# Kernel optimization log

Hardware: AMD Instinct MI355X
Metric: run time of the kernel (lower is better)

## Reference

```python
import jax, jax.numpy as jnp
import numpy as np

BASE = 257
HASH_MOD = 4096
WINDOWS = (2, 4, 8, 16)
MATCH_OFFSETS = (1, 2, 4, 8)
CHUNK = 32
EPS_LN = 1e-5


def _shift_right(x, k):
    # (B,T) -> shifted right by k along time, zero-filled
    B, T = x.shape
    return jnp.concatenate([jnp.zeros((B, k), x.dtype), x[:, :T - k]], axis=1)


def _rolling_hashes(chars):
    # polynomial rolling hash over each window size, mod HASH_MOD -> (B,T,S) int32
    c = chars.astype(jnp.int32)
    hs = []
    for w in WINDOWS:
        acc = jnp.zeros_like(c)
        p = 1
        for j in range(w):  # small fixed loop (<=16)
            acc = acc + _shift_right(c, j) * p
            p = (p * BASE) % HASH_MOD
        hs.append(acc % HASH_MOD)
    return jnp.stack(hs, axis=2)


def _match_features(chars):
    feats = []
    for k in MATCH_OFFSETS:
        m = (chars == _shift_right(chars, k)).astype(jnp.float32)
        m = m.at[:, :k].set(0.0)
        feats.append(m)
    return jnp.stack(feats, axis=-1)  # (B,T,n_match)


def _layer_norm(x, g, b):
    mu = jnp.mean(x, axis=-1, keepdims=True)
    var = jnp.mean((x - mu) ** 2, axis=-1, keepdims=True)
    return (x - mu) * jax.lax.rsqrt(var + EPS_LN) * g + b


def _forward(chars, emb_byte, hash_tables, Wq, bq, conv_w, conv_b, Win, b_in,
             Wg, bg, Wi, bi, Wo, bo, ln_g, ln_b, mlp_w, mlp_b, Wout, bout):
    B, T = chars.shape
    byte_emb = emb_byte[chars]                       # (B,T,Eb)
    hidx = _rolling_hashes(chars)                    # (B,T,S)
    scale_embeds = jnp.stack(
        [hash_tables[s][hidx[:, :, s]] for s in range(len(WINDOWS))], axis=2
    )                                                # (B,T,S,E)
    # scale attention: query from byte embedding, softmax over scales
    E = scale_embeds.shape[-1]
    q = byte_emb @ Wq + bq                           # (B,T,E)
    scores = jnp.einsum('bte,btse->bts', q, scale_embeds) / jnp.sqrt(jnp.float32(E))
    w = jax.nn.softmax(scores, axis=-1)
    hash_feat = jnp.einsum('bts,btse->bte', w, scale_embeds)
    # causal depthwise conv + silu
    C = hash_feat.shape[-1]
    kk = conv_w.shape[-1]
    ht = jnp.moveaxis(hash_feat, 1, 2)               # (B,C,T)
    ht = jnp.pad(ht, ((0, 0), (0, 0), (kk - 1, 0)))
    ht = jax.lax.conv_general_dilated(
        ht, conv_w, window_strides=(1,), padding='VALID',
        dimension_numbers=('NCH', 'OIH', 'NCH'), feature_group_count=C)
    hash_feat = jax.nn.silu(jnp.moveaxis(ht + conv_b[None, :, None], 2, 1))
    mf = _match_features(chars)
    feat = jnp.concatenate([byte_emb, hash_feat, mf], axis=-1)
    h = jax.nn.silu(feat @ Win + b_in)               # (B,T,H)
    # TinyScan: chunked log-space gated scan, carry across chunks via lax.scan
    gates = jax.nn.sigmoid(h @ Wg + bg)              # (B,T,S)
    drive = (1.0 - gates) * (h @ Wi + bi)
    S = gates.shape[-1]
    nC = T // CHUNK
    g = gates.reshape(B, nC, CHUNK, S).transpose(1, 0, 2, 3)
    d = drive.reshape(B, nC, CHUNK, S).transpose(1, 0, 2, 3)

    def step(hc, ab):
        a, b = ab                                    # (B,K,S)
        log_a = jnp.log(jnp.maximum(a, 1e-6))
        cum_a = jnp.exp(jnp.cumsum(log_a, axis=1))
        inv = 1.0 / jnp.maximum(cum_a, 1e-8)
        cum_wb = jnp.cumsum(b * inv, axis=1)
        out = cum_a * (hc[:, None, :] + cum_wb)
        return out[:, -1], out

    _, states = jax.lax.scan(step, jnp.zeros((B, S), h.dtype), (g, d))
    states = states.transpose(1, 0, 2, 3).reshape(B, T, S)
    h = _layer_norm(h + states @ Wo + bo, ln_g, ln_b)
    # residual MLP blocks: x + silu(Linear(x))
    for l in range(mlp_w.shape[0]):
        h = h + jax.nn.silu(h @ mlp_w[l] + mlp_b[l])
    return h @ Wout + bout                           # (B,T,V)


def setup_inputs() -> dict:
    key = jax.random.key(0)
    ks = jax.random.split(key, 12)
    B, T, V = 8, 8192, 256
    EB, E, H, SS, KC, NM, NR = 64, 64, 512, 32, 4, 4, 3
    feat = EB + E + NM

    def lin(k, i, o):
        return (jax.random.normal(k, (i, o), jnp.float32) / np.sqrt(i)).astype(jnp.float32)

    return {
        'chars': jax.random.randint(ks[0], (B, T), 0, V),
        'emb_byte': jax.random.normal(ks[1], (V, EB), jnp.float32) * 0.02,
        'hash_tables': jax.random.normal(ks[2], (len(WINDOWS), HASH_MOD, E), jnp.float32) * 0.02,
        'Wq': lin(ks[3], EB, E), 'bq': jnp.zeros((E,), jnp.float32),
        'conv_w': jax.random.normal(ks[4], (E, 1, KC), jnp.float32) * 0.2,
        'conv_b': jnp.zeros((E,), jnp.float32),
        'Win': lin(ks[5], feat, H), 'b_in': jnp.zeros((H,), jnp.float32),
        'Wg': lin(ks[6], H, SS), 'bg': jnp.zeros((SS,), jnp.float32),
        'Wi': lin(ks[7], H, SS), 'bi': jnp.zeros((SS,), jnp.float32),
        'Wo': lin(ks[8], SS, H), 'bo': jnp.zeros((H,), jnp.float32),
        'ln_g': jnp.ones((H,), jnp.float32), 'ln_b': jnp.zeros((H,), jnp.float32),
        'mlp_w': jax.random.normal(ks[9], (NR, H, H), jnp.float32) / np.sqrt(H),
        'mlp_b': jnp.zeros((NR, H), jnp.float32),
        'Wout': lin(ks[10], H, V), 'bout': jnp.zeros((V,), jnp.float32),
    }


def reference(chars, emb_byte, hash_tables, Wq, bq, conv_w, conv_b, Win, b_in,
              Wg, bg, Wi, bi, Wo, bo, ln_g, ln_b, mlp_w, mlp_b, Wout, bout):
    return _forward(chars, emb_byte, hash_tables, Wq, bq, conv_w, conv_b, Win, b_in,
                    Wg, bg, Wi, bi, Wo, bo, ln_g, ln_b, mlp_w, mlp_b, Wout, bout)
```

## Files before the change

### kernel.cpp

```cpp
#include <hip/hip_runtime.h>
#include <hip/hip_bf16.h>
#include <math.h>

#define B_ 8
#define T_ 8192
#define V_ 256
#define EB_ 64
#define E_ 64
#define H_ 512
#define SS_ 32
#define FEATP_ 192
#define NCH_ 256
#define CHUNK_ 32

typedef __attribute__((ext_vector_type(8))) short bf8;
typedef __attribute__((ext_vector_type(16))) float accv;

#define AS1(p) (__attribute__((address_space(1))) void*)(void*)(p)
#define AS3(p) (__attribute__((address_space(3))) void*)(void*)(p)

__device__ __forceinline__ float silu_f(float x) { return x / (1.0f + expf(-x)); }
__device__ __forceinline__ float sigm_f(float x) { return 1.0f / (1.0f + expf(-x)); }
__device__ __forceinline__ float bf2f(__hip_bfloat16 v) { return __bfloat162float(v); }
__device__ __forceinline__ __hip_bfloat16 f2bf(float v) { return __float2bfloat16(v); }
__device__ __forceinline__ float us2f(ushort u) {
    union { float f; unsigned int u32; } c; c.u32 = ((unsigned int)u) << 16; return c.f;
}
__device__ __forceinline__ ushort f2us(float v) {
    __hip_bfloat16 t = __float2bfloat16(v);
    return *reinterpret_cast<ushort*>(&t);
}

#define CD_ROW(r, lane) (((r) & 3) + 8 * ((r) >> 2) + 4 * ((lane) >> 5))

__device__ __forceinline__ int xcd_swz(int bid, int nwg) {
    return (bid & 7) * (nwg >> 3) + (bid >> 3);
}

template <int KD>
__device__ __forceinline__ void mm256(const ushort* __restrict__ Ab,
                                      const ushort* __restrict__ Bb,
                                      int m0, int n0, accv (&acc)[4][2]) {
    constexpr int NT = KD / 64;
    __shared__ __align__(1024) ushort lA[33280];
    __shared__ __align__(1024) ushort lB[33280];
    const int tid  = threadIdx.x;
    const int lane = tid & 63;
    const int w    = tid >> 6;
    const int wm   = w >> 2, wn = w & 3;
    const int l31  = lane & 31, lh = lane >> 5;

    const int srow = lane >> 3;
    const int scg  = (lane & 7) ^ ((srow & 1) << 2);
    const ushort* gA = Ab + (size_t)(m0 + w * 32 + srow) * KD + scg * 8;
    const ushort* gB = Bb + (size_t)(n0 + w * 32 + srow) * KD + scg * 8;
    const int dgrp = w * 4;

    const int rbase = (l31 >> 3) * 520 + (l31 & 7) * 64;
    int oK[4];
#pragma unroll
    for (int ks = 0; ks < 4; ks++) oK[ks] = (((ks * 2 + lh) ^ ((l31 & 1) << 2)) << 3);
    const int aoff = wm * 8320 + rbase;
    const int boff = wn * 4160 + rbase;

#define STG8(slot, kt)                                                                             \
    do {                                                                                           \
        __builtin_amdgcn_global_load_lds(AS1(gA + (kt)),                                           \
                                         AS3(&lA[(slot) * 16640 + (dgrp + 0) * 520]), 16, 0, 0);   \
        __builtin_amdgcn_global_load_lds(AS1(gB + (kt)),                                           \
                                         AS3(&lB[(slot) * 16640 + (dgrp + 0) * 520]), 16, 0, 0);   \
        __builtin_amdgcn_global_load_lds(AS1(gA + (size_t)8 * KD + (kt)),                          \
                                         AS3(&lA[(slot) * 16640 + (dgrp + 1) * 520]), 16, 0, 0);   \
        __builtin_amdgcn_global_load_lds(AS1(gB + (size_t)8 * KD + (kt)),                          \
                                         AS3(&lB[(slot) * 16640 + (dgrp + 1) * 520]), 16, 0, 0);   \
        __builtin_amdgcn_global_load_lds(AS1(gA + (size_t)16 * KD + (kt)),                         \
                                         AS3(&lA[(slot) * 16640 + (dgrp + 2) * 520]), 16, 0, 0);   \
        __builtin_amdgcn_global_load_lds(AS1(gB + (size_t)16 * KD + (kt)),                         \
                                         AS3(&lB[(slot) * 16640 + (dgrp + 2) * 520]), 16, 0, 0);   \
        __builtin_amdgcn_global_load_lds(AS1(gA + (size_t)24 * KD + (kt)),                         \
                                         AS3(&lA[(slot) * 16640 + (dgrp + 3) * 520]), 16, 0, 0);   \
        __builtin_amdgcn_global_load_lds(AS1(gB + (size_t)24 * KD + (kt)),                         \
                                         AS3(&lB[(slot) * 16640 + (dgrp + 3) * 520]), 16, 0, 0);   \
    } while (0)

#define PH(slot, ks)                                                                               \
    do {                                                                                           \
        const ushort* pa = &lA[(slot) * 16640 + aoff + oK[ks]];                                    \
        const ushort* pb = &lB[(slot) * 16640 + boff + oK[ks]];                                    \
        bf8 b0v = *(const bf8*)(pb);                                                               \
        bf8 b1v = *(const bf8*)(pb + 2080);                                                        \
        bf8 a0v = *(const bf8*)(pa);                                                               \
        bf8 a1v = *(const bf8*)(pa + 2080);                                                        \
        bf8 a2v = *(const bf8*)(pa + 4160);                                                        \
        bf8 a3v = *(const bf8*)(pa + 6240);                                                        \
        acc[0][0] = __builtin_amdgcn_mfma_f32_32x32x16_bf16(a0v, b0v, acc[0][0], 0, 0, 0);         \
        acc[0][1] = __builtin_amdgcn_mfma_f32_32x32x16_bf16(a0v, b1v, acc[0][1], 0, 0, 0);         \
        acc[1][0] = __builtin_amdgcn_mfma_f32_32x32x16_bf16(a1v, b0v, acc[1][0], 0, 0, 0);         \
        acc[1][1] = __builtin_amdgcn_mfma_f32_32x32x16_bf16(a1v, b1v, acc[1][1], 0, 0, 0);         \
        acc[2][0] = __builtin_amdgcn_mfma_f32_32x32x16_bf16(a2v, b0v, acc[2][0], 0, 0, 0);         \
        acc[2][1] = __builtin_amdgcn_mfma_f32_32x32x16_bf16(a2v, b1v, acc[2][1], 0, 0, 0);         \
        acc[3][0] = __builtin_amdgcn_mfma_f32_32x32x16_bf16(a3v, b0v, acc[3][0], 0, 0, 0);         \
        acc[3][1] = __builtin_amdgcn_mfma_f32_32x32x16_bf16(a3v, b1v, acc[3][1], 0, 0, 0);         \
    } while (0)

    STG8(0, 0);
#pragma unroll
    for (int t = 0; t < NT - 1; ++t) {
        const int slot = t & 1;
        STG8(slot ^ 1, (t + 1) * 64);
        asm volatile("s_waitcnt vmcnt(8)" ::: "memory");
        __builtin_amdgcn_s_barrier();
        __builtin_amdgcn_sched_barrier(0);
        __builtin_amdgcn_s_setprio(1);
        PH(slot, 0); PH(slot, 1); PH(slot, 2); PH(slot, 3);
        __builtin_amdgcn_s_setprio(0);
        __builtin_amdgcn_s_barrier();
    }
    asm volatile("s_waitcnt vmcnt(0)" ::: "memory");
    __builtin_amdgcn_s_barrier();
    __builtin_amdgcn_sched_barrier(0);
    {
        const int ls = (NT - 1) & 1;
        __builtin_amdgcn_s_setprio(1);
        PH(ls, 0); PH(ls, 1); PH(ls, 2); PH(ls, 3);
        __builtin_amdgcn_s_setprio(0);
    }
#undef STG8
#undef PH
}

__device__ __forceinline__ void zero_acc8(accv (&acc)[4][2]) {
#pragma unroll
    for (int i = 0; i < 4; i++)
#pragma unroll
        for (int j = 0; j < 2; j++)
#pragma unroll
            for (int r = 0; r < 16; r++) acc[i][j][r] = 0.0f;
}

__global__ __launch_bounds__(512, 2) void k_mlp256(const __hip_bfloat16* __restrict__ hin,
                                                   const __hip_bfloat16* __restrict__ Wt,
                                                   const float* __restrict__ bias,
                                                   __hip_bfloat16* __restrict__ hout) {
    accv acc[4][2];
    zero_acc8(acc);
    int wg = xcd_swz(blockIdx.x, 512);
    int m0 = (wg >> 1) * 256, n0 = (wg & 1) * 256;
    int lane = threadIdx.x & 63, w = threadIdx.x >> 6, wm = w >> 2, wn = w & 3;
    mm256<H_>((const ushort*)hin, (const ushort*)Wt, m0, n0, acc);
#pragma unroll
    for (int fr = 0; fr < 4; fr++)
#pragma unroll
        for (int fc = 0; fc < 2; fc++) {
            int col = n0 + 64 * wn + 32 * fc + (lane & 31);
            float bv = bias[col];
#pragma unroll
            for (int r = 0; r < 16; r++) {
                int row = m0 + 128 * wm + 32 * fr + CD_ROW(r, lane);
                float v = acc[fr][fc][r] + bv;
                float res = bf2f(hin[(size_t)row * H_ + col]);
                hout[(size_t)row * H_ + col] = f2bf(res + silu_f(v));
            }
        }
}

__global__ __launch_bounds__(512, 2) void k_win256(const __hip_bfloat16* __restrict__ featb,
                                                   const __hip_bfloat16* __restrict__ Wt,
                                                   const float* __restrict__ bias,
                                                   __hip_bfloat16* __restrict__ hb) {
    accv acc[4][2];
    zero_acc8(acc);
    int wg = xcd_swz(blockIdx.x, 512);
    int m0 = (wg >> 1) * 256, n0 = (wg & 1) * 256;
    int lane = threadIdx.x & 63, w = threadIdx.x >> 6, wm = w >> 2, wn = w & 3;
    mm256<FEATP_>((const ushort*)featb, (const ushort*)Wt, m0, n0, acc);
#pragma unroll
    for (int fr = 0; fr < 4; fr++)
#pragma unroll
        for (int fc = 0; fc < 2; fc++) {
            int col = n0 + 64 * wn + 32 * fc + (lane & 31);
            float bv = bias[col];
#pragma unroll
            for (int r = 0; r < 16; r++) {
                int row = m0 + 128 * wm + 32 * fr + CD_ROW(r, lane);
                hb[(size_t)row * H_ + col] = f2bf(silu_f(acc[fr][fc][r] + bv));
            }
        }
}

__global__ __launch_bounds__(512, 2) void k_out256(const __hip_bfloat16* __restrict__ hb,
                                                   const __hip_bfloat16* __restrict__ Wt,
                                                   const float* __restrict__ bout,
                                                   float* __restrict__ out) {
    accv acc[4][2];
    zero_acc8(acc);
    int wg = xcd_swz(blockIdx.x, 256);
    int m0 = wg * 256;
    int lane = threadIdx.x & 63, w = threadIdx.x >> 6, wm = w >> 2, wn = w & 3;
    mm256<H_>((const ushort*)hb, (const ushort*)Wt, m0, 0, acc);
#pragma unroll
    for (int fr = 0; fr < 4; fr++)
#pragma unroll
        for (int fc = 0; fc < 2; fc++) {
            int col = 64 * wn + 32 * fc + (lane & 31);
            float bv = bout[col];
#pragma unroll
            for (int r = 0; r < 16; r++) {
                int row = m0 + 128 * wm + 32 * fr + CD_ROW(r, lane);
                out[(size_t)row * V_ + col] = acc[fr][fc][r] + bv;
            }
        }
}

template <int KD>
__device__ __forceinline__ void mm128(const __hip_bfloat16* __restrict__ A,
                                      const __hip_bfloat16* __restrict__ Wt,
                                      int m0, int n0, accv (&acc)[2][2]) {
    __shared__ __align__(16) ushort lA[128 * 32];
    __shared__ __align__(16) ushort lB[128 * 32];
    int tid = threadIdx.x;
    int lane = tid & 63, w = tid >> 6;
    int wm = w & 1, wn = w >> 1;
    int c0 = w * 128 + lane;
    int c1 = c0 + 64;
    const ushort* Ab = (const ushort*)A;
    const ushort* Bb = (const ushort*)Wt;
    const ushort* gA0 = Ab + (size_t)(m0 + (c0 >> 2)) * KD + (c0 & 3) * 8;
    const ushort* gA1 = Ab + (size_t)(m0 + (c1 >> 2)) * KD + (c1 & 3) * 8;
    const ushort* gB0 = Bb + (size_t)(n0 + (c0 >> 2)) * KD + (c0 & 3) * 8;
    const ushort* gB1 = Bb + (size_t)(n0 + (c1 >> 2)) * KD + (c1 & 3) * 8;
    ushort* dA0 = &lA[(w * 128) * 8];
    ushort* dA1 = &lA[(w * 128 + 64) * 8];
    ushort* dB0 = &lB[(w * 128) * 8];
    ushort* dB1 = &lB[(w * 128 + 64) * 8];
    const ushort* pa = &lA[(64 * wm + (lane & 31)) * 32 + (lane >> 5) * 8];
    const ushort* pb = &lB[(64 * wn + (lane & 31)) * 32 + (lane >> 5) * 8];

    for (int kt = 0; kt < KD; kt += 32) {
        __builtin_amdgcn_global_load_lds(AS1(gA0 + kt), AS3(dA0), 16, 0, 0);
        __builtin_amdgcn_global_load_lds(AS1(gA1 + kt), AS3(dA1), 16, 0, 0);
        __builtin_amdgcn_global_load_lds(AS1(gB0 + kt), AS3(dB0), 16, 0, 0);
        __builtin_amdgcn_global_load_lds(AS1(gB1 + kt), AS3(dB1), 16, 0, 0);
        __syncthreads();
#pragma unroll
        for (int ks = 0; ks < 2; ks++) {
            bf8 a0 = *(const bf8*)(pa + ks * 16);
            bf8 a1 = *(const bf8*)(pa + 32 * 32 + ks * 16);
            bf8 b0 = *(const bf8*)(pb + ks * 16);
            bf8 b1 = *(const bf8*)(pb + 32 * 32 + ks * 16);
            acc[0][0] = __builtin_amdgcn_mfma_f32_32x32x16_bf16(a0, b0, acc[0][0], 0, 0, 0);
            acc[0][1] = __builtin_amdgcn_mfma_f32_32x32x16_bf16(a0, b1, acc[0][1], 0, 0, 0);
            acc[1][0] = __builtin_amdgcn_mfma_f32_32x32x16_bf16(a1, b0, acc[1][0], 0, 0, 0);
            acc[1][1] = __builtin_amdgcn_mfma_f32_32x32x16_bf16(a1, b1, acc[1][1], 0, 0, 0);
        }
        __syncthreads();
    }
}

__device__ __forceinline__ void zero_acc(accv (&acc)[2][2]) {
#pragma unroll
    for (int i = 0; i < 2; i++)
#pragma unroll
        for (int j = 0; j < 2; j++)
#pragma unroll
            for (int r = 0; r < 16; r++) acc[i][j][r] = 0.0f;
}

__global__ __launch_bounds__(256) void k_womm(const __hip_bfloat16* __restrict__ states_bf,
                                              const __hip_bfloat16* __restrict__ Wt_wo,
                                              const float* __restrict__ bo,
                                              const __hip_bfloat16* __restrict__ hb,
                                              __hip_bfloat16* __restrict__ tmp) {
    accv acc[2][2];
    zero_acc(acc);
    int lane = threadIdx.x & 63, w = threadIdx.x >> 6, wm = w & 1, wn = w >> 1;
    int m0 = blockIdx.x * 128, n0 = blockIdx.y * 128;
    mm128<SS_>(states_bf, Wt_wo, m0, n0, acc);
#pragma unroll
    for (int i = 0; i < 2; i++)
#pragma unroll
        for (int j = 0; j < 2; j++) {
            int col = n0 + 64 * wn + 32 * j + (lane & 31);
            float bv = bo[col];
#pragma unroll
            for (int r = 0; r < 16; r++) {
                int row = m0 + 64 * wm + 32 * i + CD_ROW(r, lane);
                float res = bf2f(hb[(size_t)row * H_ + col]);
                tmp[(size_t)row * H_ + col] = f2bf(res + acc[i][j][r] + bv);
            }
        }
}

__global__ __launch_bounds__(256) void k_ln(const __hip_bfloat16* __restrict__ tmp,
                                            const float* __restrict__ ln_g,
                                            const float* __restrict__ ln_b,
                                            __hip_bfloat16* __restrict__ hb) {
    int wave = threadIdx.x >> 6, lane = threadIdx.x & 63;
    int token = blockIdx.x * 4 + wave;
    const ushort* row = (const ushort*)(tmp + (size_t)token * H_) + lane * 8;
    bf8 xv = *(const bf8*)row;
    float x[8];
    float sm = 0.f, sq = 0.f;
#pragma unroll
    for (int i = 0; i < 8; i++) {
        x[i] = us2f((ushort)xv[i]);
        sm += x[i];
        sq += x[i] * x[i];
    }
#pragma unroll
    for (int off = 32; off; off >>= 1) {
        sm += __shfl_xor(sm, off, 64);
        sq += __shfl_xor(sq, off, 64);
    }
    float mu = sm * (1.0f / 512.0f);
    float var = sq * (1.0f / 512.0f) - mu * mu;
    float rstd = rsqrtf(fmaxf(var, 0.0f) + 1e-5f);
    float4 g0 = *(const float4*)(ln_g + lane * 8);
    float4 g1 = *(const float4*)(ln_g + lane * 8 + 4);
    float4 b0 = *(const float4*)(ln_b + lane * 8);
    float4 b1 = *(const float4*)(ln_b + lane * 8 + 4);
    float gg[8] = {g0.x, g0.y, g0.z, g0.w, g1.x, g1.y, g1.z, g1.w};
    float bb[8] = {b0.x, b0.y, b0.z, b0.w, b1.x, b1.y, b1.z, b1.w};
    bf8 o;
#pragma unroll
    for (int i = 0; i < 8; i++) o[i] = (short)f2us((x[i] - mu) * rstd * gg[i] + bb[i]);
    *(bf8*)((ushort*)(hb + (size_t)token * H_) + lane * 8) = o;
}

__global__ __launch_bounds__(256) void k_gates_mfma(const __hip_bfloat16* __restrict__ hb,
                                                    const __hip_bfloat16* __restrict__ Wt_gd,
                                                    const float* __restrict__ bg,
                                                    const float* __restrict__ bi,
                                                    float* __restrict__ gates,
                                                    float* __restrict__ drive) {
    __shared__ __align__(16) ushort lA[256 * 32];
    __shared__ __align__(16) ushort lB[64 * 32];
    int tid = threadIdx.x, lane = tid & 63, w = tid >> 6;
    int m0 = blockIdx.x * 256;
    accv acc[2][2];
    zero_acc(acc);
    const ushort* Ab = (const ushort*)hb;
    const ushort* Bb = (const ushort*)Wt_gd;
    const ushort* pa = &lA[(64 * w + (lane & 31)) * 32 + (lane >> 5) * 8];
    const ushort* pb = &lB[((lane & 31)) * 32 + (lane >> 5) * 8];
    int cb = w * 64 + lane;
    const ushort* gB = Bb + (size_t)(cb >> 2) * H_ + (cb & 3) * 8;
    for (int kt = 0; kt < H_; kt += 32) {
#pragma unroll
        for (int j = 0; j < 4; j++) {
            int c = w * 256 + j * 64 + lane;
            __builtin_amdgcn_global_load_lds(
                AS1(Ab + (size_t)(m0 + (c >> 2)) * H_ + (c & 3) * 8 + kt),
                AS3(&lA[(w * 256 + j * 64) * 8]), 16, 0, 0);
        }
        __builtin_amdgcn_global_load_lds(AS1(gB + kt), AS3(&lB[(w * 64) * 8]), 16, 0, 0);
        __syncthreads();
#pragma unroll
        for (int ks = 0; ks < 2; ks++) {
            bf8 a0 = *(const bf8*)(pa + ks * 16);
            bf8 a1 = *(const bf8*)(pa + 32 * 32 + ks * 16);
            bf8 b0 = *(const bf8*)(pb + ks * 16);
            bf8 b1 = *(const bf8*)(pb + 32 * 32 + ks * 16);
            acc[0][0] = __builtin_amdgcn_mfma_f32_32x32x16_bf16(a0, b0, acc[0][0], 0, 0, 0);
            acc[0][1] = __builtin_amdgcn_mfma_f32_32x32x16_bf16(a0, b1, acc[0][1], 0, 0, 0);
            acc[1][0] = __builtin_amdgcn_mfma_f32_32x32x16_bf16(a1, b0, acc[1][0], 0, 0, 0);
            acc[1][1] = __builtin_amdgcn_mfma_f32_32x32x16_bf16(a1, b1, acc[1][1], 0, 0, 0);
        }
        __syncthreads();
    }
    int c = lane & 31;
    float bgv = bg[c], biv = bi[c];
#pragma unroll
    for (int i = 0; i < 2; i++)
#pragma unroll
        for (int r = 0; r < 16; r++) {
            int row = m0 + 64 * w + 32 * i + CD_ROW(r, lane);
            float g = sigm_f(acc[i][0][r] + bgv);
            float d = (1.0f - g) * (acc[i][1][r] + biv);
            gates[(size_t)row * SS_ + c] = g;
            drive[(size_t)row * SS_ + c] = d;
        }
}

__global__ __launch_bounds__(256) void k_prep_w(const float* __restrict__ mlp_w,
                                                const float* __restrict__ Wout,
                                                const float* __restrict__ Win,
                                                const float* __restrict__ Wg,
                                                const float* __restrict__ Wi,
                                                const float* __restrict__ Wo,
                                                const float* __restrict__ Wq,
                                                const float* __restrict__ bq,
                                                const float* __restrict__ emb_byte,
                                                __hip_bfloat16* __restrict__ Wt_mlp,
                                                __hip_bfloat16* __restrict__ Wt_out,
                                                __hip_bfloat16* __restrict__ Wt_win,
                                                __hip_bfloat16* __restrict__ Wt_gd,
                                                __hip_bfloat16* __restrict__ Wt_wo,
                                                float* __restrict__ Qtab) {
    int idx = blockIdx.x * 256 + threadIdx.x;
    if (idx < 786432) {
        int l = idx >> 18, rem = idx & 262143;
        int n = rem >> 9, k = rem & 511;
        Wt_mlp[idx] = f2bf(mlp_w[l * 262144 + k * 512 + n]);
    } else if (idx < 917504) {
        int rem = idx - 786432;
        int n = rem >> 9, k = rem & 511;
        Wt_out[rem] = f2bf(Wout[k * 256 + n]);
    } else if (idx < 1015808) {
        int rem = idx - 917504;
        int n = rem / FEATP_, k = rem % FEATP_;
        Wt_win[rem] = f2bf(k < 132 ? Win[k * 512 + n] : 0.0f);
    } else if (idx < 1048576) {
        int rem = idx - 1015808;
        int n = rem >> 9, k = rem & 511;
        Wt_gd[rem] = f2bf(n < 32 ? Wg[k * 32 + n] : Wi[k * 32 + (n - 32)]);
    } else if (idx < 1064960) {
        int rem = idx - 1048576;
        int n = rem >> 5, k = rem & 31;
        Wt_wo[rem] = f2bf(Wo[k * H_ + n]);
    } else if (idx < 1081344) {
        int rem = idx - 1064960;
        int c = rem >> 6, e = rem & 63;
        float a = bq[e];
#pragma unroll 8
        for (int k = 0; k < 64; k++) a += emb_byte[c * 64 + k] * Wq[k * 64 + e];
        Qtab[rem] = a * 0.125f;
    }
}

__global__ __launch_bounds__(256) void k_token_feats(
    const int* __restrict__ chars, const float* __restrict__ emb_byte,
    const float* __restrict__ hash_tables, const float* __restrict__ Qtab,
    __hip_bfloat16* __restrict__ featb, float* __restrict__ hfpre) {
    int wave = threadIdx.x >> 6, lane = threadIdx.x & 63;
    int token = blockIdx.x * 4 + wave;
    int t = token & (T_ - 1);
    int b = token >> 13;
    const int* crow = chars + b * T_;
    int cv[16];
#pragma unroll
    for (int j = 0; j < 16; j++) cv[j] = (t >= j) ? crow[t - j] : 0;
    int acc = 0;
    int hidx[4];
#pragma unroll
    for (int j = 0; j < 16; j++) {
        acc += cv[j] * (1 + 256 * j);
        if (j == 1) hidx[0] = acc & 4095;
        if (j == 3) hidx[1] = acc & 4095;
        if (j == 7) hidx[2] = acc & 4095;
        if (j == 15) hidx[3] = acc & 4095;
    }
    int c0 = cv[0];
    float be = emb_byte[c0 * EB_ + lane];
    float q = Qtab[c0 * 64 + lane];
    float se[4];
#pragma unroll
    for (int s = 0; s < 4; s++) se[s] = hash_tables[(s * 4096 + hidx[s]) * E_ + lane];
    float sc[4];
#pragma unroll
    for (int s = 0; s < 4; s++) {
        float v = q * se[s];
#pragma unroll
        for (int off = 32; off; off >>= 1) v += __shfl_xor(v, off, 64);
        sc[s] = v;
    }
    float mx = fmaxf(fmaxf(sc[0], sc[1]), fmaxf(sc[2], sc[3]));
    float w0 = expf(sc[0] - mx), w1 = expf(sc[1] - mx), w2 = expf(sc[2] - mx), w3 = expf(sc[3] - mx);
    float inv = 1.0f / (w0 + w1 + w2 + w3);
    float hf = (w0 * se[0] + w1 * se[1] + w2 * se[2] + w3 * se[3]) * inv;
    featb[(size_t)token * FEATP_ + lane] = f2bf(be);
    hfpre[(size_t)token * E_ + lane] = hf;
    if (lane < 32) {
        float m = 0.0f;
        if (lane < 4) {
            int k = 1 << lane;
            m = (t >= k && c0 == cv[k]) ? 1.0f : 0.0f;
        }
        featb[(size_t)token * FEATP_ + 128 + lane] = f2bf(m);
    } else {
        featb[(size_t)token * FEATP_ + 128 + lane] = f2bf(0.0f);
    }
}

__global__ __launch_bounds__(256) void k_conv(
    const float* __restrict__ hfpre, const float* __restrict__ conv_w,
    const float* __restrict__ conv_b, __hip_bfloat16* __restrict__ featb) {
    int idx = blockIdx.x * 256 + threadIdx.x;
    int e = idx & 63;
    int bt = idx >> 6;
    int t = bt & (T_ - 1);
    float acc = conv_b[e];
#pragma unroll
    for (int k = 0; k < 4; k++) {
        int tt = t - 3 + k;
        if (tt >= 0) acc += hfpre[(size_t)(bt - 3 + k) * E_ + e] * conv_w[e * 4 + k];
    }
    featb[(size_t)bt * FEATP_ + 64 + e] = f2bf(silu_f(acc));
}

__global__ __launch_bounds__(256) void k_chunk_ab(
    const float* __restrict__ gates, const float* __restrict__ drive,
    float* __restrict__ chA, float* __restrict__ chB) {
    int gid = blockIdx.x * 256 + threadIdx.x;
    int s = gid & 31;
    int n = (gid >> 5) & (NCH_ - 1);
    int b = gid >> 13;
    int base = (b * T_ + n * CHUNK_) * SS_ + s;
    float suml = 0.f, cum_wb = 0.f, cum_a = 1.f;
    for (int i = 0; i < CHUNK_; i++) {
        float g = gates[base + i * SS_];
        float d = drive[base + i * SS_];
        suml += logf(fmaxf(g, 1e-6f));
        cum_a = expf(suml);
        cum_wb += d / fmaxf(cum_a, 1e-8f);
    }
    chA[gid] = cum_a;
    chB[gid] = cum_a * cum_wb;
}

__global__ void k_chunk_scan(const float* __restrict__ chA, const float* __restrict__ chB,
                             float* __restrict__ chH) {
    int tid = threadIdx.x;
    int b = tid >> 5, s = tid & 31;
    const float* pA = chA + (size_t)b * NCH_ * SS_ + s;
    const float* pB = chB + (size_t)b * NCH_ * SS_ + s;
    float* pH = chH + (size_t)b * NCH_ * SS_ + s;
    float hc = 0.f;
    for (int n = 0; n < NCH_; n += 8) {
        float a[8], bb[8];
#pragma unroll
        for (int i = 0; i < 8; i++) {
            a[i] = pA[(n + i) * SS_];
            bb[i] = pB[(n + i) * SS_];
        }
#pragma unroll
        for (int i = 0; i < 8; i++) {
            pH[(n + i) * SS_] = hc;
            hc = a[i] * hc + bb[i];
        }
    }
}

__global__ __launch_bounds__(256) void k_states(
    const float* __restrict__ gates, const float* __restrict__ drive,
    const float* __restrict__ chH, __hip_bfloat16* __restrict__ states_bf) {
    int gid = blockIdx.x * 256 + threadIdx.x;
    int s = gid & 31;
    int n = (gid >> 5) & (NCH_ - 1);
    int b = gid >> 13;
    int base = (b * T_ + n * CHUNK_) * SS_ + s;
    float hc = chH[gid];
    float suml = 0.f, cum_wb = 0.f;
    for (int i = 0; i < CHUNK_; i++) {
        float g = gates[base + i * SS_];
        float d = drive[base + i * SS_];
        suml += logf(fmaxf(g, 1e-6f));
        float cum_a = expf(suml);
        cum_wb += d / fmaxf(cum_a, 1e-8f);
        states_bf[base + i * SS_] = f2bf(cum_a * (hc + cum_wb));
    }
}

extern "C" void kernel_launch(void* const* d_in, const int* in_sizes, int n_in,
                              void* d_out, int out_size, void* d_ws, size_t ws_size,
                              hipStream_t stream) {
    (void)in_sizes; (void)n_in; (void)out_size; (void)ws_size;
    const int*   chars       = (const int*)  d_in[0];
    const float* emb_byte    = (const float*)d_in[1];
    const float* hash_tables = (const float*)d_in[2];
    const float* Wq          = (const float*)d_in[3];
    const float* bq          = (const float*)d_in[4];
    const float* conv_w      = (const float*)d_in[5];
    const float* conv_b      = (const float*)d_in[6];
    const float* Win         = (const float*)d_in[7];
    const float* b_in        = (const float*)d_in[8];
    const float* Wg          = (const float*)d_in[9];
    const float* bg          = (const float*)d_in[10];
    const float* Wi          = (const float*)d_in[11];
    const float* bi          = (const float*)d_in[12];
    const float* Wo          = (const float*)d_in[13];
    const float* bo          = (const float*)d_in[14];
    const float* ln_g        = (const float*)d_in[15];
    const float* ln_b        = (const float*)d_in[16];
    const float* mlp_w       = (const float*)d_in[17];
    const float* mlp_b       = (const float*)d_in[18];
    const float* Wout        = (const float*)d_in[19];
    const float* bout        = (const float*)d_in[20];
    float* out = (float*)d_out;

    const size_t NTOK = (size_t)B_ * T_;
    char* p = (char*)d_ws;
    auto alloc = [&](size_t bytes) { void* r = (void*)p; p += (bytes + 255) & ~(size_t)255; return r; };
    __hip_bfloat16* featb = (__hip_bfloat16*)alloc(NTOK * FEATP_ * 2);
    float*          hfpre = (float*)alloc(NTOK * E_ * 4);
    __hip_bfloat16* hbA   = (__hip_bfloat16*)alloc(NTOK * H_ * 2);
    __hip_bfloat16* hbB   = (__hip_bfloat16*)alloc(NTOK * H_ * 2);
    float*          gates = (float*)alloc(NTOK * SS_ * 4);
    float*          drive = (float*)alloc(NTOK * SS_ * 4);
    __hip_bfloat16* states_bf = (__hip_bfloat16*)alloc(NTOK * SS_ * 2);
    float*          chA   = (float*)alloc((size_t)B_ * NCH_ * SS_ * 4);
    float*          chB   = (float*)alloc((size_t)B_ * NCH_ * SS_ * 4);
    float*          chH   = (float*)alloc((size_t)B_ * NCH_ * SS_ * 4);
    __hip_bfloat16* Wt_mlp= (__hip_bfloat16*)alloc(3 * 512 * 512 * 2);
    __hip_bfloat16* Wt_out= (__hip_bfloat16*)alloc(256 * 512 * 2);
    __hip_bfloat16* Wt_win= (__hip_bfloat16*)alloc(512 * FEATP_ * 2);
    __hip_bfloat16* Wt_gd = (__hip_bfloat16*)alloc(64 * 512 * 2);
    __hip_bfloat16* Wt_wo = (__hip_bfloat16*)alloc(512 * SS_ * 2);
    float*          Qtab  = (float*)alloc(256 * 64 * 4);

    k_prep_w<<<4224, 256, 0, stream>>>(mlp_w, Wout, Win, Wg, Wi, Wo, Wq, bq, emb_byte,
                                       Wt_mlp, Wt_out, Wt_win, Wt_gd, Wt_wo, Qtab);
    k_token_feats<<<NTOK / 4, 256, 0, stream>>>(chars, emb_byte, hash_tables, Qtab, featb, hfpre);
    k_conv<<<NTOK * E_ / 256, 256, 0, stream>>>(hfpre, conv_w, conv_b, featb);
    k_win256<<<512, 512, 0, stream>>>(featb, Wt_win, b_in, hbA);
    k_gates_mfma<<<NTOK / 256, 256, 0, stream>>>(hbA, Wt_gd, bg, bi, gates, drive);
    k_chunk_ab<<<B_ * NCH_ * SS_ / 256, 256, 0, stream>>>(gates, drive, chA, chB);
    k_chunk_scan<<<1, 256, 0, stream>>>(chA, chB, chH);
    k_states<<<B_ * NCH_ * SS_ / 256, 256, 0, stream>>>(gates, drive, chH, states_bf);
    k_womm<<<dim3(NTOK / 128, 4), 256, 0, stream>>>(states_bf, Wt_wo, bo, hbA, hbB);
    k_ln<<<NTOK / 4, 256, 0, stream>>>(hbB, ln_g, ln_b, hbA);
    k_mlp256<<<512, 512, 0, stream>>>(hbA, Wt_mlp, mlp_b, hbB);
    k_mlp256<<<512, 512, 0, stream>>>(hbB, Wt_mlp + 262144, mlp_b + 512, hbA);
    k_mlp256<<<512, 512, 0, stream>>>(hbA, Wt_mlp + 524288, mlp_b + 1024, hbB);
    k_out256<<<256, 512, 0, stream>>>(hbB, Wt_out, bout, out);
}
```

Baseline: 529.7 us.

## Fuse Wo projection, residual add and LayerNorm into one kernel

Replaces the separate MFMA Wo matmul kernel and the LayerNorm kernel with a single kernel. It stages the bf16 Wo weight in LDS, computes the K=32 projection with scalar FMAs using readlane broadcasts of the state values, adds the residual and bias, and applies LayerNorm in registers before storing. This removes the bf16 round trip of the intermediate tensor through global memory and one kernel launch. In exchange the small matmul runs on VALU instead of matrix cores, and the ping-pong buffer order of the later MLP kernels is swapped.

```diff
diff --git a/kernel.cpp b/kernel.cpp
--- a/kernel.cpp
+++ b/kernel.cpp
@@ -29,6 +29,9 @@
 __device__ __forceinline__ ushort f2us(float v) {
     __hip_bfloat16 t = __float2bfloat16(v);
     return *reinterpret_cast<ushort*>(&t);
+}
+__device__ __forceinline__ float rdlane(float v, int l) {
+    return __int_as_float(__builtin_amdgcn_readlane(__float_as_int(v), l));
 }
 
 #define CD_ROW(r, lane) (((r) & 3) + 8 * ((r) >> 2) + 4 * ((lane) >> 5))
@@ -212,119 +215,113 @@
         }
 }
 
-template <int KD>
-__device__ __forceinline__ void mm128(const __hip_bfloat16* __restrict__ A,
-                                      const __hip_bfloat16* __restrict__ Wt,
-                                      int m0, int n0, accv (&acc)[2][2]) {
-    __shared__ __align__(16) ushort lA[128 * 32];
-    __shared__ __align__(16) ushort lB[128 * 32];
-    int tid = threadIdx.x;
-    int lane = tid & 63, w = tid >> 6;
-    int wm = w & 1, wn = w >> 1;
-    int c0 = w * 128 + lane;
-    int c1 = c0 + 64;
-    const ushort* Ab = (const ushort*)A;
-    const ushort* Bb = (const ushort*)Wt;
-    const ushort* gA0 = Ab + (size_t)(m0 + (c0 >> 2)) * KD + (c0 & 3) * 8;
-    const ushort* gA1 = Ab + (size_t)(m0 + (c1 >> 2)) * KD + (c1 & 3) * 8;
-    const ushort* gB0 = Bb + (size_t)(n0 + (c0 >> 2)) * KD + (c0 & 3) * 8;
-    const ushort* gB1 = Bb + (size_t)(n0 + (c1 >> 2)) * KD + (c1 & 3) * 8;
-    ushort* dA0 = &lA[(w * 128) * 8];
-    ushort* dA1 = &lA[(w * 128 + 64) * 8];
-    ushort* dB0 = &lB[(w * 128) * 8];
-    ushort* dB1 = &lB[(w * 128 + 64) * 8];
-    const ushort* pa = &lA[(64 * wm + (lane & 31)) * 32 + (lane >> 5) * 8];
-    const ushort* pb = &lB[(64 * wn + (lane & 31)) * 32 + (lane >> 5) * 8];
-
-    for (int kt = 0; kt < KD; kt += 32) {
-        __builtin_amdgcn_global_load_lds(AS1(gA0 + kt), AS3(dA0), 16, 0, 0);
-        __builtin_amdgcn_global_load_lds(AS1(gA1 + kt), AS3(dA1), 16, 0, 0);
-        __builtin_amdgcn_global_load_lds(AS1(gB0 + kt), AS3(dB0), 16, 0, 0);
-        __builtin_amdgcn_global_load_lds(AS1(gB1 + kt), AS3(dB1), 16, 0, 0);
-        __syncthreads();
-#pragma unroll
-        for (int ks = 0; ks < 2; ks++) {
-            bf8 a0 = *(const bf8*)(pa + ks * 16);
-            bf8 a1 = *(const bf8*)(pa + 32 * 32 + ks * 16);
-            bf8 b0 = *(const bf8*)(pb + ks * 16);
-            bf8 b1 = *(const bf8*)(pb + 32 * 32 + ks * 16);
-            acc[0][0] = __builtin_amdgcn_mfma_f32_32x32x16_bf16(a0, b0, acc[0][0], 0, 0, 0);
-            acc[0][1] = __builtin_amdgcn_mfma_f32_32x32x16_bf16(a0, b1, acc[0][1], 0, 0, 0);
-            acc[1][0] = __builtin_amdgcn_mfma_f32_32x32x16_bf16(a1, b0, acc[1][0], 0, 0, 0);
-            acc[1][1] = __builtin_amdgcn_mfma_f32_32x32x16_bf16(a1, b1, acc[1][1], 0, 0, 0);
-        }
-        __syncthreads();
-    }
-}
-
-__device__ __forceinline__ void zero_acc(accv (&acc)[2][2]) {
-#pragma unroll
-    for (int i = 0; i < 2; i++)
-#pragma unroll
-        for (int j = 0; j < 2; j++)
-#pragma unroll
-            for (int r = 0; r < 16; r++) acc[i][j][r] = 0.0f;
-}
-
-__global__ __launch_bounds__(256) void k_womm(const __hip_bfloat16* __restrict__ states_bf,
-                                              const __hip_bfloat16* __restrict__ Wt_wo,
-                                              const float* __restrict__ bo,
-                                              const __hip_bfloat16* __restrict__ hb,
-                                              __hip_bfloat16* __restrict__ tmp) {
-    accv acc[2][2];
-    zero_acc(acc);
-    int lane = threadIdx.x & 63, w = threadIdx.x >> 6, wm = w & 1, wn = w >> 1;
-    int m0 = blockIdx.x * 128, n0 = blockIdx.y * 128;
-    mm128<SS_>(states_bf, Wt_wo, m0, n0, acc);
-#pragma unroll
-    for (int i = 0; i < 2; i++)
-#pragma unroll
-        for (int j = 0; j < 2; j++) {
-            int col = n0 + 64 * wn + 32 * j + (lane & 31);
-            float bv = bo[col];
-#pragma unroll
-            for (int r = 0; r < 16; r++) {
-                int row = m0 + 64 * wm + 32 * i + CD_ROW(r, lane);
-                float res = bf2f(hb[(size_t)row * H_ + col]);
-                tmp[(size_t)row * H_ + col] = f2bf(res + acc[i][j][r] + bv);
-            }
-        }
-}
-
-__global__ __launch_bounds__(256) void k_ln(const __hip_bfloat16* __restrict__ tmp,
-                                            const float* __restrict__ ln_g,
-                                            const float* __restrict__ ln_b,
-                                            __hip_bfloat16* __restrict__ hb) {
-    int wave = threadIdx.x >> 6, lane = threadIdx.x & 63;
-    int token = blockIdx.x * 4 + wave;
-    const ushort* row = (const ushort*)(tmp + (size_t)token * H_) + lane * 8;
-    bf8 xv = *(const bf8*)row;
-    float x[8];
-    float sm = 0.f, sq = 0.f;
-#pragma unroll
-    for (int i = 0; i < 8; i++) {
-        x[i] = us2f((ushort)xv[i]);
-        sm += x[i];
-        sq += x[i] * x[i];
-    }
-#pragma unroll
-    for (int off = 32; off; off >>= 1) {
-        sm += __shfl_xor(sm, off, 64);
-        sq += __shfl_xor(sq, off, 64);
-    }
-    float mu = sm * (1.0f / 512.0f);
-    float var = sq * (1.0f / 512.0f) - mu * mu;
-    float rstd = rsqrtf(fmaxf(var, 0.0f) + 1e-5f);
+__global__ __launch_bounds__(512) void k_wln(
+    const __hip_bfloat16* __restrict__ states_bf,
+    const __hip_bfloat16* __restrict__ Wo2,
+    const float* __restrict__ bo,
+    const __hip_bfloat16* __restrict__ h_in,
+    const float* __restrict__ ln_g,
+    const float* __restrict__ ln_b,
+    __hip_bfloat16* __restrict__ h_out) {
+    __shared__ __align__(1024) ushort lW[16384];
+    const int tid = threadIdx.x, lane = tid & 63, w = tid >> 6;
+
+    {
+        const ushort* srcw = (const ushort*)Wo2 + w * 2048 + lane * 8;
+        ushort* dstw = &lW[w * 2048];
+#pragma unroll
+        for (int i = 0; i < 4; ++i)
+            __builtin_amdgcn_global_load_lds(AS1(srcw + i * 512), AS3(dstw + i * 512), 16, 0, 0);
+    }
+
     float4 g0 = *(const float4*)(ln_g + lane * 8);
     float4 g1 = *(const float4*)(ln_g + lane * 8 + 4);
-    float4 b0 = *(const float4*)(ln_b + lane * 8);
-    float4 b1 = *(const float4*)(ln_b + lane * 8 + 4);
+    float4 lb0 = *(const float4*)(ln_b + lane * 8);
+    float4 lb1 = *(const float4*)(ln_b + lane * 8 + 4);
+    float4 bo0 = *(const float4*)(bo + lane * 8);
+    float4 bo1 = *(const float4*)(bo + lane * 8 + 4);
     float gg[8] = {g0.x, g0.y, g0.z, g0.w, g1.x, g1.y, g1.z, g1.w};
-    float bb[8] = {b0.x, b0.y, b0.z, b0.w, b1.x, b1.y, b1.z, b1.w};
-    bf8 o;
-#pragma unroll
-    for (int i = 0; i < 8; i++) o[i] = (short)f2us((x[i] - mu) * rstd * gg[i] + bb[i]);
-    *(bf8*)((ushort*)(hb + (size_t)token * H_) + lane * 8) = o;
+    float bbv[8] = {lb0.x, lb0.y, lb0.z, lb0.w, lb1.x, lb1.y, lb1.z, lb1.w};
+    float bov[8] = {bo0.x, bo0.y, bo0.z, bo0.w, bo1.x, bo1.y, bo1.z, bo1.w};
+
+    asm volatile("s_waitcnt vmcnt(0)" ::: "memory");
+    __syncthreads();
+
+    const ushort* Sb = (const ushort*)states_bf;
+    const ushort* Hb = (const ushort*)h_in;
+    ushort* Ob = (ushort*)h_out;
+
+    for (int pass = 0; pass < 2; ++pass) {
+        const int tok0 = blockIdx.x * 64 + pass * 32 + w * 4;
+        const ushort* s0 = Sb + (size_t)tok0 * 32;
+        float svA = us2f(s0[lane]);
+        float svB = us2f(s0[64 + lane]);
+        const ushort* h0 = Hb + (size_t)tok0 * 512 + lane * 8;
+        float a0[8], a1[8], a2[8], a3[8];
+        {
+            uint4 u0 = *(const uint4*)(h0);
+            uint4 u1 = *(const uint4*)(h0 + 512);
+            uint4 u2 = *(const uint4*)(h0 + 1024);
+            uint4 u3 = *(const uint4*)(h0 + 1536);
+#define UNP(dst, u)                                                                  \
+            dst[0] = __uint_as_float(u.x << 16) + bov[0];                            \
+            dst[1] = __uint_as_float(u.x & 0xffff0000u) + bov[1];                    \
+            dst[2] = __uint_as_float(u.y << 16) + bov[2];                            \
+            dst[3] = __uint_as_float(u.y & 0xffff0000u) + bov[3];                    \
+            dst[4] = __uint_as_float(u.z << 16) + bov[4];                            \
+            dst[5] = __uint_as_float(u.z & 0xffff0000u) + bov[5];                    \
+            dst[6] = __uint_as_float(u.w << 16) + bov[6];                            \
+            dst[7] = __uint_as_float(u.w & 0xffff0000u) + bov[7];
+            UNP(a0, u0) UNP(a1, u1) UNP(a2, u2) UNP(a3, u3)
+#undef UNP
+        }
+#pragma unroll
+        for (int k = 0; k < 32; ++k) {
+            uint4 wu = *(const uint4*)&lW[k * 512 + lane * 8];
+            float wf[8];
+            wf[0] = __uint_as_float(wu.x << 16);
+            wf[1] = __uint_as_float(wu.x & 0xffff0000u);
+            wf[2] = __uint_as_float(wu.y << 16);
+            wf[3] = __uint_as_float(wu.y & 0xffff0000u);
+            wf[4] = __uint_as_float(wu.z << 16);
+            wf[5] = __uint_as_float(wu.z & 0xffff0000u);
+            wf[6] = __uint_as_float(wu.w << 16);
+            wf[7] = __uint_as_float(wu.w & 0xffff0000u);
+            float s0k = rdlane(svA, k);
+            float s1k = rdlane(svA, 32 + k);
+            float s2k = rdlane(svB, k);
+            float s3k = rdlane(svB, 32 + k);
+#pragma unroll
+            for (int j = 0; j < 8; ++j) {
+                a0[j] = fmaf(s0k, wf[j], a0[j]);
+                a1[j] = fmaf(s1k, wf[j], a1[j]);
+                a2[j] = fmaf(s2k, wf[j], a2[j]);
+                a3[j] = fmaf(s3k, wf[j], a3[j]);
+            }
+        }
+        auto ln_store = [&](float (&ax)[8], int tok) {
+            float sm = 0.f, sq = 0.f;
+#pragma unroll
+            for (int j = 0; j < 8; ++j) { sm += ax[j]; sq += ax[j] * ax[j]; }
+#pragma unroll
+            for (int off = 32; off; off >>= 1) {
+                sm += __shfl_xor(sm, off, 64);
+                sq += __shfl_xor(sq, off, 64);
+            }
+            float mu = sm * (1.0f / 512.0f);
+            float var = sq * (1.0f / 512.0f) - mu * mu;
+            float rstd = rsqrtf(fmaxf(var, 0.0f) + 1e-5f);
+            bf8 o;
+#pragma unroll
+            for (int j = 0; j < 8; ++j)
+                o[j] = (short)f2us((ax[j] - mu) * rstd * gg[j] + bbv[j]);
+            *(bf8*)(Ob + (size_t)tok * 512 + lane * 8) = o;
+        };
+        ln_store(a0, tok0);
+        ln_store(a1, tok0 + 1);
+        ln_store(a2, tok0 + 2);
+        ln_store(a3, tok0 + 3);
+    }
 }
 
 __global__ __launch_bounds__(256) void k_gates_mfma(const __hip_bfloat16* __restrict__ hb,
@@ -338,7 +335,12 @@
     int tid = threadIdx.x, lane = tid & 63, w = tid >> 6;
     int m0 = blockIdx.x * 256;
     accv acc[2][2];
-    zero_acc(acc);
+#pragma unroll
+    for (int i = 0; i < 2; i++)
+#pragma unroll
+        for (int j = 0; j < 2; j++)
+#pragma unroll
+            for (int r = 0; r < 16; r++) acc[i][j][r] = 0.0f;
     const ushort* Ab = (const ushort*)hb;
     const ushort* Bb = (const ushort*)Wt_gd;
     const ushort* pa = &lA[(64 * w + (lane & 31)) * 32 + (lane >> 5) * 8];
@@ -396,7 +398,8 @@
                                                 __hip_bfloat16* __restrict__ Wt_win,
                                                 __hip_bfloat16* __restrict__ Wt_gd,
                                                 __hip_bfloat16* __restrict__ Wt_wo,
-                                                float* __restrict__ Qtab) {
+                                                float* __restrict__ Qtab,
+                                                __hip_bfloat16* __restrict__ Wt_wo2) {
     int idx = blockIdx.x * 256 + threadIdx.x;
     if (idx < 786432) {
         int l = idx >> 18, rem = idx & 262143;
@@ -425,6 +428,9 @@
 #pragma unroll 8
         for (int k = 0; k < 64; k++) a += emb_byte[c * 64 + k] * Wq[k * 64 + e];
         Qtab[rem] = a * 0.125f;
+    } else if (idx < 1097728) {
+        int rem = idx - 1081344;
+        Wt_wo2[rem] = f2bf(Wo[rem]);
     }
 }
 
@@ -607,9 +613,10 @@
     __hip_bfloat16* Wt_gd = (__hip_bfloat16*)alloc(64 * 512 * 2);
     __hip_bfloat16* Wt_wo = (__hip_bfloat16*)alloc(512 * SS_ * 2);
     float*          Qtab  = (float*)alloc(256 * 64 * 4);
-
-    k_prep_w<<<4224, 256, 0, stream>>>(mlp_w, Wout, Win, Wg, Wi, Wo, Wq, bq, emb_byte,
-                                       Wt_mlp, Wt_out, Wt_win, Wt_gd, Wt_wo, Qtab);
+    __hip_bfloat16* Wt_wo2= (__hip_bfloat16*)alloc(32 * 512 * 2);
+
+    k_prep_w<<<4288, 256, 0, stream>>>(mlp_w, Wout, Win, Wg, Wi, Wo, Wq, bq, emb_byte,
+                                       Wt_mlp, Wt_out, Wt_win, Wt_gd, Wt_wo, Qtab, Wt_wo2);
     k_token_feats<<<NTOK / 4, 256, 0, stream>>>(chars, emb_byte, hash_tables, Qtab, featb, hfpre);
     k_conv<<<NTOK * E_ / 256, 256, 0, stream>>>(hfpre, conv_w, conv_b, featb);
     k_win256<<<512, 512, 0, stream>>>(featb, Wt_win, b_in, hbA);
@@ -617,10 +624,9 @@
     k_chunk_ab<<<B_ * NCH_ * SS_ / 256, 256, 0, stream>>>(gates, drive, chA, chB);
     k_chunk_scan<<<1, 256, 0, stream>>>(chA, chB, chH);
     k_states<<<B_ * NCH_ * SS_ / 256, 256, 0, stream>>>(gates, drive, chH, states_bf);
-    k_womm<<<dim3(NTOK / 128, 4), 256, 0, stream>>>(states_bf, Wt_wo, bo, hbA, hbB);
-    k_ln<<<NTOK / 4, 256, 0, stream>>>(hbB, ln_g, ln_b, hbA);
-    k_mlp256<<<512, 512, 0, stream>>>(hbA, Wt_mlp, mlp_b, hbB);
-    k_mlp256<<<512, 512, 0, stream>>>(hbB, Wt_mlp + 262144, mlp_b + 512, hbA);
-    k_mlp256<<<512, 512, 0, stream>>>(hbA, Wt_mlp + 524288, mlp_b + 1024, hbB);
-    k_out256<<<256, 512, 0, stream>>>(hbB, Wt_out, bout, out);
-}
+    k_wln<<<NTOK / 64, 512, 0, stream>>>(states_bf, Wt_wo2, bo, hbA, ln_g, ln_b, hbB);
+    k_mlp256<<<512, 512, 0, stream>>>(hbB, Wt_mlp, mlp_b, hbA);
+    k_mlp256<<<512, 512, 0, stream>>>(hbA, Wt_mlp + 262144, mlp_b + 512, hbB);
+    k_mlp256<<<512, 512, 0, stream>>>(hbB, Wt_mlp + 524288, mlp_b + 1024, hbA);
+    k_out256<<<256, 512, 0, stream>>>(hbA, Wt_out, bout, out);
+}
```

Result: slower. 1.103 ms (+108.3%).
